# Kernel optimization log

Measured on AMD Instinct MI355X. Metric: run time of the kernel, lower is better.

The kernel has to match this reference:

```python
import jax, jax.numpy as jnp
import numpy as np
import math

B, L, D_MODEL = 4, 2048, 512
EXPAND, D_STATE, D_CONV = 6, 8, 3
D_INNER = EXPAND * D_MODEL            # 3072
DT_RANK = math.ceil(D_MODEL / 16)     # 32
NH = 8
HF = D_MODEL // NH                    # 64


def setup_inputs() -> dict:
    key = jax.random.key(0)
    ks = jax.random.split(key, 16)
    n = lambda k, sh, s=0.02: jax.random.normal(k, sh, dtype=jnp.float32) * s
    return {
        "x": jax.random.normal(ks[0], (B, L, D_MODEL), dtype=jnp.float32),
        "norm_w": jnp.ones((D_MODEL,), jnp.float32),
        "in_proj_w": n(ks[1], (2 * D_INNER, D_MODEL)),
        "conv_w": n(ks[2], (D_INNER, 1, D_CONV), 0.2),
        "conv_b": jnp.zeros((D_INNER,), jnp.float32),
        "x_proj_w": n(ks[3], (DT_RANK + 2 * D_STATE, D_INNER)),
        "dt_head_w": n(ks[4], (D_INNER, DT_RANK)),
        "dt_head_b": jnp.zeros((D_INNER,), jnp.float32),
        "D": jnp.ones((D_INNER,), jnp.float32),
        "reduce_w": n(ks[5], (D_MODEL, D_INNER)),
        "q_net_w": n(ks[6], (D_MODEL, D_MODEL)),
        "gain_q_w": n(ks[7], (D_MODEL, D_MODEL)),
        "gain_k_w": n(ks[8], (D_MODEL, D_MODEL)),
        "alpha": jnp.ones((1,), jnp.float32),
        "beta": jnp.zeros((1,), jnp.float32),
        "qkv_w": n(ks[9], (3 * D_MODEL + NH, D_MODEL)),
        "qkv_b": jnp.zeros((3 * D_MODEL + NH,), jnp.float32),
        "ttt_lr_bias": jnp.zeros((NH,), jnp.float32),
        "W1": n(ks[10], (NH, HF, HF)),
        "b1": jnp.zeros((NH, HF), jnp.float32),
        "token_idx": 1.0 / jnp.arange(1, L + 1, dtype=jnp.float32),
        "token_idx_bias": jnp.zeros((L,), jnp.float32),
        "ttt_ln_w": jnp.ones((NH, HF), jnp.float32),
        "ttt_ln_b": jnp.zeros((NH, HF), jnp.float32),
        "post_norm_w": jnp.ones((D_MODEL,), jnp.float32),
        "post_norm_b": jnp.zeros((D_MODEL,), jnp.float32),
        "wo_w": n(ks[11], (D_MODEL, D_MODEL)),
        "wo_b": jnp.zeros((D_MODEL,), jnp.float32),
    }


def _rmsnorm(x, w, eps=1e-5):
    return x * jax.lax.rsqrt(jnp.mean(x * x, axis=-1, keepdims=True) + eps) * w


def _layernorm(x, w, b, eps=1e-5):
    mu = x.mean(-1, keepdims=True)
    xh = (x - mu) * jax.lax.rsqrt(x.var(-1, keepdims=True) + eps)
    return xh * w + b


def _longhorn_scan(x, z, dt, k, q, dt_b, D):
    # x,z,dt: [B,L,di]; k,q: [B,L,ds].  Online Longhorn recurrence (matches step()).
    def step(s, t):
        x_t, z_t, dt_t, k_t, q_t = t
        dt_t = jax.nn.sigmoid(dt_t + dt_b)
        dt_t = dt_t / (1.0 + dt_t * jnp.sum(k_t * k_t, -1, keepdims=True))
        dB = dt_t[:, :, None] * k_t[:, None, :]                  # [B,di,ds]
        s = s * (1.0 - dB * k_t[:, None, :]) + x_t[:, :, None] * dB
        y_t = jnp.einsum('bdn,bn->bd', s, q_t) + D * x_t
        return s, y_t * jax.nn.silu(z_t)

    s0 = jnp.zeros((x.shape[0], x.shape[2], k.shape[2]), x.dtype)
    xs = tuple(jnp.moveaxis(a, 1, 0) for a in (x, z, dt, k, q))
    _, ys = jax.lax.scan(step, s0, xs)
    return jnp.moveaxis(ys, 0, 1)                                # [B,L,di]


def _ttt(h, qkv_w, qkv_b, ttt_lr_bias, W1, b1, token_idx, token_idx_bias,
         ln_w, ln_b, pn_w, pn_b, wo_w, wo_b, lr_mult=1.0):
    Bh, N, d = h.shape
    proj = h @ qkv_w.T + qkv_b                                   # [B,N,3d+NH]
    XQK, XV, XGate, lr = (proj[..., :d], proj[..., d:2 * d],
                          proj[..., 2 * d:3 * d], proj[..., 3 * d:])

    def heads(a):  # [B,N,d] -> [B*NH,N,HF]
        return a.reshape(Bh, N, NH, HF).transpose(0, 2, 1, 3).reshape(Bh * NH, N, HF)

    XQ = heads(XQK)            # XQ == XK in the source
    XVh = heads(XV)
    ttt_lr = jax.nn.sigmoid(lr + ttt_lr_bias) * lr_mult          # [B,N,NH]
    ttt_lr = jnp.swapaxes(ttt_lr, 0, 1).reshape(N, Bh * NH, 1)   # [N,B*NH,1]
    tok = jnp.maximum(token_idx + token_idx_bias, 0.0)           # [N]

    W1c = jnp.broadcast_to(W1[None], (Bh, NH, HF, HF)).reshape(Bh * NH, HF, HF)
    b1c = jnp.broadcast_to(b1[None], (Bh, NH, HF)).reshape(Bh * NH, HF)
    lnw = jnp.broadcast_to(ln_w[None], (Bh, NH, HF)).reshape(Bh * NH, HF)
    lnb = jnp.broadcast_to(ln_b[None], (Bh, NH, HF)).reshape(Bh * NH, HF)
    eps = 1e-6
    HFf = jnp.float32(HF)

    def step(carry, t):
        W, bb = carry
        xk, xv, lr_t, tok_t = t
        Z1 = jnp.einsum('bf,bfg->bg', xk, W) + bb
        mu = Z1.mean(-1, keepdims=True)
        std = jnp.sqrt(Z1.var(-1, keepdims=True) + eps)
        xh = (Z1 - mu) / std
        # grad of ||LN(Z1) - (XV - XK)||^2 wrt Z1 (ln_fused_l2_bwd)
        go = (lnw * xh + lnb) - (xv - xk)
        gxh = go * lnw
        grad = (HFf * gxh - gxh.sum(-1, keepdims=True)
                - xh * (gxh * xh).sum(-1, keepdims=True)) / (HFf * std)
        eta = lr_t * tok_t                                       # [B*NH,1]
        W = W - eta[:, :, None] * (xk[:, :, None] * grad[:, None, :])
        bb = bb - eta * grad
        Z1q = jnp.einsum('bf,bfg->bg', xk, W) + bb
        mu2 = Z1q.mean(-1, keepdims=True)
        std2 = jnp.sqrt(Z1q.var(-1, keepdims=True) + eps)
        out_t = xk + lnw * (Z1q - mu2) / std2 + lnb
        return (W, bb), out_t

    xs = (jnp.moveaxis(XQ, 1, 0), jnp.moveaxis(XVh, 1, 0), ttt_lr, tok)
    _, ys = jax.lax.scan(step, (W1c, b1c), xs)                   # [N,B*NH,HF]
    xqw = ys.reshape(N, Bh, NH, HF).transpose(1, 0, 2, 3).reshape(Bh, N, d)
    normed = _layernorm(xqw, pn_w, pn_b)
    gated = jax.nn.gelu(XGate, approximate=True) * normed
    return gated @ wo_w.T + wo_b


def reference(x, norm_w, in_proj_w, conv_w, conv_b, x_proj_w, dt_head_w, dt_head_b,
              D, reduce_w, q_net_w, gain_q_w, gain_k_w, alpha, beta,
              qkv_w, qkv_b, ttt_lr_bias, W1, b1, token_idx, token_idx_bias,
              ttt_ln_w, ttt_ln_b, post_norm_w, post_norm_b, wo_w, wo_b):
    residual = x                                   # residual=None in forward
    xn = _rmsnorm(residual, norm_w)
    # ---- Longhorn block ----
    xz = xn @ in_proj_w.T                          # [B,L,2*di]
    xx, z = jnp.split(xz, 2, axis=-1)
    xc = jnp.swapaxes(xx, 1, 2)                    # [B,di,L]
    xc = jax.lax.conv_general_dilated(
        xc, conv_w, (1,), [(D_CONV - 1, 0)],       # causal depthwise conv
        dimension_numbers=('NCH', 'OIH', 'NCH'), feature_group_count=D_INNER)
    xc = jax.nn.silu(xc + conv_b[None, :, None])
    xb = jnp.swapaxes(xc, 1, 2)                    # [B,L,di]
    x_dbl = xb @ x_proj_w.T
    dt = x_dbl[..., :DT_RANK] @ dt_head_w.T        # [B,L,di] (bias added in scan)
    k = x_dbl[..., DT_RANK:DT_RANK + D_STATE]
    q = x_dbl[..., DT_RANK + D_STATE:]
    y = _longhorn_scan(xb, z, dt, k, q, dt_head_b, D)   # h_hidden, [B,L,di]
    # (out_proj output is discarded by PreCoBlock, so not computed)
    h_red = y @ reduce_w.T                          # [B,L,d]
    # ---- TTT corrective branch ----
    c_hidden = _ttt(h_red, qkv_w, qkv_b, ttt_lr_bias, W1, b1, token_idx,
                    token_idx_bias, ttt_ln_w, ttt_ln_b, post_norm_w, post_norm_b,
                    wo_w, wo_b, lr_mult=1.0)
    z_long = h_red @ q_net_w.T
    z_ttt = c_hidden @ q_net_w.T
    gq = h_red @ gain_q_w.T
    gk = h_red @ gain_k_w.T
    # score = mean_i (gq_i . gk_j)/sqrt(d) == (mean_i gq_i) . gk_j / sqrt(d)
    score = jnp.einsum('bd,bld->bl', gq.mean(axis=1), gk) / jnp.sqrt(jnp.float32(D_MODEL))
    gain = jnp.minimum(jax.nn.sigmoid(alpha * score + beta), 0.55)[..., None]
    out = z_long + gain * (z_ttt - z_long)
    return (out, residual, gain)
```

## Files before the change

kernel.cpp:

```cpp
#include <hip/hip_runtime.h>
#include <hip/hip_bf16.h>
#include <cstdint>
#include <cstddef>

#define L_SEQ 2048
#define BATCH 4
#define DM    512
#define DI    3072
#define NROWS (BATCH * L_SEQ)
#define PROJW 1544
#define CTILE 16
#define BDI   (BATCH * DI)
#define SB    64
#define NSB   (L_SEQ / SB)
#define CHT   16
#define LCH   256
#define NLCH  (L_SEQ / LCH)

using bf16 = __hip_bfloat16;

typedef __attribute__((ext_vector_type(8))) short short8v;
typedef __attribute__((ext_vector_type(4))) float f32x4;


__device__ __forceinline__ float sigmoidf_(float x) { return 1.f / (1.f + __expf(-x)); }
__device__ __forceinline__ float us2f(unsigned int u) {
    union { unsigned int i; float f; } c; c.i = u << 16; return c.f;
}
__device__ __forceinline__ bf16  f2b(float f) { return __float2bfloat16(f); }
__device__ __forceinline__ float b2f(bf16 v)  { return __bfloat162float(v); }
__device__ __forceinline__ void st1(float* p, float v) { *p = v; }
__device__ __forceinline__ void st1(bf16* p, float v)  { *p = f2b(v); }

template <int CTRL>
__device__ __forceinline__ float dppadd_(float x) {
    int s = __builtin_amdgcn_update_dpp(0, __builtin_bit_cast(int, x), CTRL, 0xF, 0xF, true);
    return x + __builtin_bit_cast(float, s);
}
__device__ __forceinline__ float wave_sum_u(float x) {
    x = dppadd_<0x111>(x);
    x = dppadd_<0x112>(x);
    x = dppadd_<0x114>(x);
    x = dppadd_<0x118>(x);
    x = dppadd_<0x142>(x);
    x = dppadd_<0x143>(x);
    return __builtin_bit_cast(float,
        __builtin_amdgcn_readlane(__builtin_bit_cast(int, x), 63));
}

__global__ __launch_bounds__(256) void copy4_k(const float4* __restrict__ in,
                                               float4* __restrict__ out, int n) {
    int i = blockIdx.x * 256 + threadIdx.x;
    if (i < n) out[i] = in[i];
}

__global__ __launch_bounds__(256) void cvt_k(const float* __restrict__ in,
                                             bf16* __restrict__ out, int n4) {
    int i = blockIdx.x * 256 + threadIdx.x;
    if (i >= n4) return;
    float4 v = ((const float4*)in)[i];
    out[4 * i + 0] = f2b(v.x);
    out[4 * i + 1] = f2b(v.y);
    out[4 * i + 2] = f2b(v.z);
    out[4 * i + 3] = f2b(v.w);
}

#define C_RED  393216
#define C_QKV  197632
#define C_WO   65536
#define C_XP   73728
#define C_W1   65536
__global__ __launch_bounds__(256) void cvt_all_k(const float* __restrict__ reduce_w,
                                                 const float* __restrict__ qkv_w,
                                                 const float* __restrict__ wo_w,
                                                 const float* __restrict__ xproj_w,
                                                 const float* __restrict__ qnet_w,
                                                 const float* __restrict__ gainq_w,
                                                 const float* __restrict__ gaink_w,
                                                 bf16* __restrict__ redb,
                                                 bf16* __restrict__ qkvb,
                                                 bf16* __restrict__ wob,
                                                 bf16* __restrict__ xpb,
                                                 bf16* __restrict__ wcat) {
    int i = blockIdx.x * 256 + threadIdx.x;
    const float* src;
    bf16* dst;
    int j;
    if (i < C_RED)                { src = reduce_w; dst = redb;  j = i; }
    else if (i < C_RED + C_QKV)   { src = qkv_w;    dst = qkvb;  j = i - C_RED; }
    else if (i < C_RED + C_QKV + C_WO) { src = wo_w; dst = wob;  j = i - C_RED - C_QKV; }
    else if (i < C_RED + C_QKV + C_WO + C_XP) { src = xproj_w; dst = xpb; j = i - C_RED - C_QKV - C_WO; }
    else if (i < C_RED + C_QKV + C_WO + C_XP + C_W1) { src = qnet_w; dst = wcat; j = i - C_RED - C_QKV - C_WO - C_XP; }
    else if (i < C_RED + C_QKV + C_WO + C_XP + 2 * C_W1) { src = gainq_w; dst = wcat + (size_t)C_W1 * 4; j = i - C_RED - C_QKV - C_WO - C_XP - C_W1; }
    else if (i < C_RED + C_QKV + C_WO + C_XP + 3 * C_W1) { src = gaink_w; dst = wcat + (size_t)2 * C_W1 * 4; j = i - C_RED - C_QKV - C_WO - C_XP - 2 * C_W1; }
    else return;
    float4 v = ((const float4*)src)[j];
    bf16* o = dst + (size_t)j * 4;
    o[0] = f2b(v.x); o[1] = f2b(v.y); o[2] = f2b(v.z); o[3] = f2b(v.w);
}

__global__ __launch_bounds__(256) void rmsnorm_res_k(const float* __restrict__ x,
                                                     const float* __restrict__ w,
                                                     bf16* __restrict__ xn,
                                                     float* __restrict__ res) {
    int r = blockIdx.x, tid = threadIdx.x;
    const float* row = x + (size_t)r * DM;
    float v0 = row[tid], v1 = row[tid + 256];
    float q = v0 * v0 + v1 * v1;
#pragma unroll
    for (int off = 32; off; off >>= 1) q += __shfl_xor(q, off);
    __shared__ float sm[4];
    if ((tid & 63) == 0) sm[tid >> 6] = q;
    __syncthreads();
    q = sm[0] + sm[1] + sm[2] + sm[3];
    float scale = rsqrtf(q * (1.f / 512.f) + 1e-5f);
    bf16* orow = xn + (size_t)r * DM;
    float* rrow = res + (size_t)r * DM;
    orow[tid]       = f2b(v0 * scale * w[tid]);
    orow[tid + 256] = f2b(v1 * scale * w[tid + 256]);
    rrow[tid]       = v0;
    rrow[tid + 256] = v1;
}

template <int BIAS, typename TC>
__global__ __launch_bounds__(256) void gemm_mfma(const bf16* __restrict__ A, int lda,
                                                 const bf16* __restrict__ Wb, int ldw,
                                                 const float* __restrict__ bias,
                                                 TC* __restrict__ C, int ldc,
                                                 int N, int K) {
    __shared__ __align__(16) bf16 As[128 * 48];
    __shared__ __align__(16) bf16 Ws[128 * 48];
    const int tid = threadIdx.x;
    const int lane = tid & 63;
    const int widx = tid >> 6;
    const int bm = blockIdx.x * 128;
    const int bn = blockIdx.y * 128;
    const int wr = (widx >> 1) * 64;
    const int wc = (widx & 1) * 64;

    f32x4 acc[4][4];
#pragma unroll
    for (int i = 0; i < 4; ++i)
#pragma unroll
        for (int j = 0; j < 4; ++j) acc[i][j] = (f32x4){0.f, 0.f, 0.f, 0.f};

    const int r0 = tid >> 2;
    const int c0 = tid & 3;
    const int frow = lane & 15;
    const int fk = (lane >> 4) * 8;

    int n0 = bn + r0;       if (n0 > N - 1) n0 = N - 1;
    int n1 = bn + r0 + 64;  if (n1 > N - 1) n1 = N - 1;
    const bf16* pa0 = A + (size_t)(bm + r0) * lda + c0 * 8;
    const bf16* pa1 = A + (size_t)(bm + r0 + 64) * lda + c0 * 8;
    const bf16* pb0 = Wb + (size_t)n0 * ldw + c0 * 8;
    const bf16* pb1 = Wb + (size_t)n1 * ldw + c0 * 8;

    for (int k0 = 0; k0 < K; k0 += 32) {
        short8v a0 = *(const short8v*)(pa0 + k0);
        short8v a1 = *(const short8v*)(pa1 + k0);
        short8v b0 = *(const short8v*)(pb0 + k0);
        short8v b1 = *(const short8v*)(pb1 + k0);
        __syncthreads();
        *(short8v*)&As[r0 * 48 + c0 * 8] = a0;
        *(short8v*)&As[(r0 + 64) * 48 + c0 * 8] = a1;
        *(short8v*)&Ws[r0 * 48 + c0 * 8] = b0;
        *(short8v*)&Ws[(r0 + 64) * 48 + c0 * 8] = b1;
        __syncthreads();
        short8v af[4], bg[4];
#pragma unroll
        for (int mi = 0; mi < 4; ++mi)
            af[mi] = *(const short8v*)&As[(wr + mi * 16 + frow) * 48 + fk];
#pragma unroll
        for (int ni = 0; ni < 4; ++ni)
            bg[ni] = *(const short8v*)&Ws[(wc + ni * 16 + frow) * 48 + fk];
#pragma unroll
        for (int mi = 0; mi < 4; ++mi)
#pragma unroll
            for (int ni = 0; ni < 4; ++ni)
                acc[mi][ni] = __builtin_amdgcn_mfma_f32_16x16x32_bf16(
                    af[mi], bg[ni], acc[mi][ni], 0, 0, 0);
    }

#pragma unroll
    for (int ni = 0; ni < 4; ++ni) {
        int col = bn + wc + ni * 16 + (lane & 15);
        if (col < N) {
            float bz = BIAS ? bias[col] : 0.f;
#pragma unroll
            for (int mi = 0; mi < 4; ++mi) {
                int rbase = bm + wr + mi * 16 + (lane >> 4) * 4;
#pragma unroll
                for (int r = 0; r < 4; ++r) {
                    float v = acc[mi][ni][r] + bz;
                    st1(&C[(size_t)(rbase + r) * ldc + col], v);
                }
            }
        }
    }
}

__global__ __launch_bounds__(256) void gemm_inproj(const bf16* __restrict__ A,
                                                   const bf16* __restrict__ Wb,
                                                   bf16* __restrict__ cx,
                                                   bf16* __restrict__ cz) {
    __shared__ __align__(16) bf16 As[128 * 48];
    __shared__ __align__(16) bf16 Ws[128 * 48];
    const int tid = threadIdx.x;
    const int lane = tid & 63;
    const int widx = tid >> 6;
    const int bm = blockIdx.x * 128;
    const int bn = blockIdx.y * 128;
    const int wr = (widx >> 1) * 64;
    const int wc = (widx & 1) * 64;

    f32x4 acc[4][4];
#pragma unroll
    for (int i = 0; i < 4; ++i)
#pragma unroll
        for (int j = 0; j < 4; ++j) acc[i][j] = (f32x4){0.f, 0.f, 0.f, 0.f};

    const int r0 = tid >> 2;
    const int c0 = tid & 3;
    const int frow = lane & 15;
    const int fk = (lane >> 4) * 8;

    const bf16* pa0 = A + (size_t)(bm + r0) * DM + c0 * 8;
    const bf16* pa1 = A + (size_t)(bm + r0 + 64) * DM + c0 * 8;
    const bf16* pb0 = Wb + (size_t)(bn + r0) * DM + c0 * 8;
    const bf16* pb1 = Wb + (size_t)(bn + r0 + 64) * DM + c0 * 8;

    for (int k0 = 0; k0 < DM; k0 += 32) {
        short8v a0 = *(const short8v*)(pa0 + k0);
        short8v a1 = *(const short8v*)(pa1 + k0);
        short8v b0 = *(const short8v*)(pb0 + k0);
        short8v b1 = *(const short8v*)(pb1 + k0);
        __syncthreads();
        *(short8v*)&As[r0 * 48 + c0 * 8] = a0;
        *(short8v*)&As[(r0 + 64) * 48 + c0 * 8] = a1;
        *(short8v*)&Ws[r0 * 48 + c0 * 8] = b0;
        *(short8v*)&Ws[(r0 + 64) * 48 + c0 * 8] = b1;
        __syncthreads();
        short8v af[4], bg[4];
#pragma unroll
        for (int mi = 0; mi < 4; ++mi)
            af[mi] = *(const short8v*)&As[(wr + mi * 16 + frow) * 48 + fk];
#pragma unroll
        for (int ni = 0; ni < 4; ++ni)
            bg[ni] = *(const short8v*)&Ws[(wc + ni * 16 + frow) * 48 + fk];
#pragma unroll
        for (int mi = 0; mi < 4; ++mi)
#pragma unroll
            for (int ni = 0; ni < 4; ++ni)
                acc[mi][ni] = __builtin_amdgcn_mfma_f32_16x16x32_bf16(
                    af[mi], bg[ni], acc[mi][ni], 0, 0, 0);
    }

    bf16* Cb = (bn < DI) ? cx : cz;
    const int coff = (bn < DI) ? 0 : DI;
#pragma unroll
    for (int ni = 0; ni < 4; ++ni) {
        int col = bn + wc + ni * 16 + (lane & 15) - coff;
#pragma unroll
        for (int mi = 0; mi < 4; ++mi) {
            int rbase = bm + wr + mi * 16 + (lane >> 4) * 4;
#pragma unroll
            for (int r = 0; r < 4; ++r)
                Cb[(size_t)(rbase + r) * DI + col] = f2b(acc[mi][ni][r]);
        }
    }
}

__global__ __launch_bounds__(256) void conv_boundary_k(const bf16* __restrict__ x,
                                                       bf16* __restrict__ side) {
    int idx = blockIdx.x * 256 + threadIdx.x;
    const int total = (L_SEQ / CTILE - 1) * 2 * BDI;
    if (idx >= total) return;
    int col = idx % BDI;
    int rr = idx / BDI;
    int tile = (rr >> 1) + 1;
    int r = rr & 1;
    int b = col / DI, d = col % DI;
    int l = tile * CTILE - 2 + r;
    side[idx] = x[((size_t)b * L_SEQ + l) * DI + d];
}

__global__ __launch_bounds__(256) void conv_tile_k(bf16* __restrict__ x,
                                                   const bf16* __restrict__ side,
                                                   const float* __restrict__ cw,
                                                   const float* __restrict__ cb) {
    int idx = blockIdx.x * 256 + threadIdx.x;
    const int total = (L_SEQ / CTILE) * BDI;
    if (idx >= total) return;
    int col = idx % BDI;
    int tile = idx / BDI;
    int b = col / DI, d = col % DI;
    float w0 = cw[3 * d], w1 = cw[3 * d + 1], w2 = cw[3 * d + 2], bias = cb[d];
    size_t base = ((size_t)b * L_SEQ + tile * CTILE) * DI + d;
    float xm2, xm1;
    if (tile == 0) { xm2 = 0.f; xm1 = 0.f; }
    else {
        const bf16* sp = side + ((size_t)(tile - 1) * 2) * BDI + col;
        xm2 = b2f(sp[0]);
        xm1 = b2f(sp[BDI]);
    }
    float cur = b2f(x[base]);
#pragma unroll
    for (int i = 0; i < CTILE; ++i) {
        float nxt = (i + 1 < CTILE) ? b2f(x[base + (size_t)(i + 1) * DI]) : 0.f;
        float a = bias + w0 * xm2 + w1 * xm1 + w2 * cur;
        x[base + (size_t)i * DI] = f2b(a * sigmoidf_(a));
        xm2 = xm1; xm1 = cur; cur = nxt;
    }
}

__global__ __launch_bounds__(256) void longhorn_p1(const bf16* __restrict__ xb,
                                                   const float* __restrict__ xdbl,
                                                   const float* __restrict__ dtw,
                                                   const float* __restrict__ dtb_v,
                                                   float* __restrict__ pq) {
    int idx = blockIdx.x * 256 + threadIdx.x;
    int ch = idx / BDI;
    int col = idx % BDI;
    int b = col / DI, d = col % DI;
    float w32[32];
#pragma unroll
    for (int i = 0; i < 32; ++i) w32[i] = dtw[d * 32 + i];
    float dtb = dtb_v[d];
    float P[8] = {1.f, 1.f, 1.f, 1.f, 1.f, 1.f, 1.f, 1.f};
    float Q[8] = {0.f, 0.f, 0.f, 0.f, 0.f, 0.f, 0.f, 0.f};
    size_t rbase = ((size_t)b * L_SEQ + ch * LCH) * DI + d;
    const float* xdb = xdbl + ((size_t)b * L_SEQ + ch * LCH) * 48;

    float xv = b2f(xb[rbase]);
    for (int t = 0; t < LCH; ++t) {
        float x_c = xv;
        if (t + 1 < LCH) xv = b2f(xb[rbase + (size_t)(t + 1) * DI]);
        const float* row = xdb + (size_t)t * 48;
        float dt_c = 0.f;
#pragma unroll
        for (int i = 0; i < 32; i += 4) {
            float4 r4 = *(const float4*)(row + i);
            dt_c = fmaf(r4.x, w32[i + 0], dt_c);
            dt_c = fmaf(r4.y, w32[i + 1], dt_c);
            dt_c = fmaf(r4.z, w32[i + 2], dt_c);
            dt_c = fmaf(r4.w, w32[i + 3], dt_c);
        }
        float kq[8];
#pragma unroll
        for (int i = 0; i < 8; i += 4) *(float4*)&kq[i] = *(const float4*)(row + 32 + i);
        float sig = sigmoidf_(dt_c + dtb);
        float ksq = 0.f;
#pragma unroll
        for (int n = 0; n < 8; ++n) ksq = fmaf(kq[n], kq[n], ksq);
        float dts = sig / (1.f + sig * ksq);
#pragma unroll
        for (int n = 0; n < 8; ++n) {
            float dB = dts * kq[n];
            float a = 1.f - dB * kq[n];
            P[n] *= a;
            Q[n] = fmaf(Q[n], a, x_c * dB);
        }
    }
    float* o = pq + (size_t)idx * 16;
#pragma unroll
    for (int n = 0; n < 8; n += 4) {
        *(float4*)(o + n)     = make_float4(P[n], P[n + 1], P[n + 2], P[n + 3]);
        *(float4*)(o + 8 + n) = make_float4(Q[n], Q[n + 1], Q[n + 2], Q[n + 3]);
    }
}

__global__ __launch_bounds__(256) void longhorn_p2(float* __restrict__ pq) {
    int col = blockIdx.x * 256 + threadIdx.x;
    float s[8] = {0.f, 0.f, 0.f, 0.f, 0.f, 0.f, 0.f, 0.f};
    for (int c = 0; c < NLCH; ++c) {
        float* base = pq + ((size_t)c * BDI + col) * 16;
        float P[8], Q[8];
#pragma unroll
        for (int n = 0; n < 8; n += 4) {
            *(float4*)&P[n] = *(const float4*)(base + n);
            *(float4*)&Q[n] = *(const float4*)(base + 8 + n);
        }
#pragma unroll
        for (int n = 0; n < 8; n += 4)
            *(float4*)(base + n) = make_float4(s[n], s[n + 1], s[n + 2], s[n + 3]);
#pragma unroll
        for (int n = 0; n < 8; ++n) s[n] = fmaf(P[n], s[n], Q[n]);
    }
}

__global__ __launch_bounds__(256) void longhorn_p3(bf16* __restrict__ xb_y,
                                                   const bf16* __restrict__ z,
                                                   const float* __restrict__ xdbl,
                                                   const float* __restrict__ dtw,
                                                   const float* __restrict__ dtb_v,
                                                   const float* __restrict__ Dv,
                                                   const float* __restrict__ pq) {
    int idx = blockIdx.x * 256 + threadIdx.x;
    int ch = idx / BDI;
    int col = idx % BDI;
    int b = col / DI, d = col % DI;
    float w32[32];
#pragma unroll
    for (int i = 0; i < 32; ++i) w32[i] = dtw[d * 32 + i];
    float dtb = dtb_v[d], Dd = Dv[d];
    float s[8];
    {
        const float* base = pq + (size_t)idx * 16;
#pragma unroll
        for (int n = 0; n < 8; n += 4) *(float4*)&s[n] = *(const float4*)(base + n);
    }
    size_t rbase = ((size_t)b * L_SEQ + ch * LCH) * DI + d;
    const float* xdb = xdbl + ((size_t)b * L_SEQ + ch * LCH) * 48;

    float xv = b2f(xb_y[rbase]);
    float zv = b2f(z[rbase]);
    for (int t = 0; t < LCH; ++t) {
        float x_c = xv, z_c = zv;
        if (t + 1 < LCH) {
            size_t nidx = rbase + (size_t)(t + 1) * DI;
            xv = b2f(xb_y[nidx]);
            zv = b2f(z[nidx]);
        }
        const float* row = xdb + (size_t)t * 48;
        float dt_c = 0.f;
#pragma unroll
        for (int i = 0; i < 32; i += 4) {
            float4 r4 = *(const float4*)(row + i);
            dt_c = fmaf(r4.x, w32[i + 0], dt_c);
            dt_c = fmaf(r4.y, w32[i + 1], dt_c);
            dt_c = fmaf(r4.z, w32[i + 2], dt_c);
            dt_c = fmaf(r4.w, w32[i + 3], dt_c);
        }
        float kq[16];
#pragma unroll
        for (int i = 0; i < 16; i += 4) *(float4*)&kq[i] = *(const float4*)(row + 32 + i);
        float sig = sigmoidf_(dt_c + dtb);
        float ksq = 0.f;
#pragma unroll
        for (int n = 0; n < 8; ++n) ksq = fmaf(kq[n], kq[n], ksq);
        float dts = sig / (1.f + sig * ksq);
        float y = 0.f;
#pragma unroll
        for (int n = 0; n < 8; ++n) {
            float dB = dts * kq[n];
            s[n] = s[n] * (1.f - dB * kq[n]) + x_c * dB;
            y = fmaf(s[n], kq[8 + n], y);
        }
        y = fmaf(Dd, x_c, y);
        float out = y * (z_c * sigmoidf_(z_c));
        xb_y[rbase + (size_t)t * DI] = f2b(out);
    }
}

__global__ __launch_bounds__(128) void prep_gram_k(const bf16* __restrict__ proj,
                                                   const float* __restrict__ lr_bias,
                                                   const float* __restrict__ tok_idx,
                                                   const float* __restrict__ tok_bias,
                                                   const float* __restrict__ ln_w,
                                                   const float* __restrict__ ln_b,
                                                   float* __restrict__ xkf,
                                                   float* __restrict__ etav,
                                                   float* __restrict__ q0s,
                                                   float* __restrict__ gram) {
    __shared__ __align__(16) float xs[128][68];
    int bh = blockIdx.x >> 4;
    int blk16 = blockIdx.x & 15;
    int tid = threadIdx.x;
    int t = blk16 * 128 + tid;
    int b = bh >> 3, h = bh & 7;
    const bf16* prow = proj + ((size_t)b * L_SEQ + t) * PROJW;
    const bf16* pk = prow + h * 64;
    const bf16* pv = prow + 512 + h * 64;
    const float* lwp = ln_w + h * 64;
    const float* lbp = ln_b + h * 64;
    float* xo = xkf + ((size_t)bh * L_SEQ + t) * 64;
    float q0 = 0.f;
#pragma unroll
    for (int i = 0; i < 64; i += 8) {
        short8v sk = *(const short8v*)(pk + i);
        short8v sv = *(const short8v*)(pv + i);
        float v[8];
#pragma unroll
        for (int j = 0; j < 8; ++j) {
            float xk = us2f((unsigned short)sk[j]);
            float xv = us2f((unsigned short)sv[j]);
            v[j] = xk;
            q0 = fmaf((lbp[i + j] - xv + xk), lwp[i + j], q0);
        }
        float4 lo = make_float4(v[0], v[1], v[2], v[3]);
        float4 hi = make_float4(v[4], v[5], v[6], v[7]);
        *(float4*)(xo + i)     = lo;
        *(float4*)(xo + i + 4) = hi;
        *(float4*)&xs[tid][i]     = lo;
        *(float4*)&xs[tid][i + 4] = hi;
    }
    float eta = sigmoidf_(b2f(prow[1536 + h]) + lr_bias[h]) *
                fmaxf(tok_idx[t] + tok_bias[t], 0.f);
    size_t o = (size_t)bh * L_SEQ + t;
    etav[o] = eta;
    q0s[o]  = q0;
    __syncthreads();
    int chunk = tid >> 4, tt = tid & 15;
    const float* rt = &xs[chunk * 16 + tt][0];
    float* dst = gram + (((size_t)bh * 128 + blk16 * 8 + chunk) * 16 + tt) * 16;
#pragma unroll
    for (int ss = 0; ss < 16; ++ss) {
        const float* rs = &xs[chunk * 16 + ss][0];
        float a0 = 0.f, a1 = 0.f, a2 = 0.f, a3 = 0.f;
#pragma unroll
        for (int j = 0; j < 16; ++j) {
            float4 u = *(const float4*)(rt + 4 * j);
            float4 v = *(const float4*)(rs + 4 * j);
            a0 = fmaf(u.x, v.x, a0); a1 = fmaf(u.y, v.y, a1);
            a2 = fmaf(u.z, v.z, a2); a3 = fmaf(u.w, v.w, a3);
        }
        dst[ss] = (a0 + a1) + (a2 + a3);
    }
}

__device__ __forceinline__ void ttt_body(const bf16* __restrict__ proj,
                                         const float* __restrict__ xkf,
                                         const float* __restrict__ etav,
                                         const float* __restrict__ q0s,
                                         const float* __restrict__ gram16,
                                         const float* __restrict__ W1,
                                         const float* __restrict__ b1,
                                         const float* __restrict__ ln_w,
                                         const float* __restrict__ ln_b,
                                         bf16* __restrict__ xqw) {
    const int lane = threadIdx.x;
    const int bh = blockIdx.x;
    const int b = bh >> 3, h = bh & 7;

    __shared__ __align__(16) float xkb[2][SB][64];
    __shared__ __align__(16) bf16  xvb[2][SB][64];
    __shared__ __align__(16) float kb[2][4][CHT][CHT];
    __shared__ __align__(16) float sc[2][2][SB];
    __shared__ __align__(16) float zbb[CHT][64];
    __shared__ __align__(16) float z1qb[CHT][64];
    __shared__ __align__(16) float egb[CHT][64];
    __shared__ float mub[CHT];

    float W[64];
#pragma unroll
    for (int f = 0; f < 64; ++f) W[f] = W1[(size_t)(h * 64 + f) * 64 + lane];
    float bvec = b1[h * 64 + lane];
    float lw = ln_w[h * 64 + lane];
    float lb = ln_b[h * 64 + lane];
    float p = lw * lw;

    const float* kfg = xkf + (size_t)bh * L_SEQ * 64;
    const bf16*  pvg = proj + (size_t)b * L_SEQ * PROJW + 512 + h * 64;
    const float* evg = etav + (size_t)bh * L_SEQ;
    const float* qg  = q0s + (size_t)bh * L_SEQ;
    const float* gmg = gram16 + (size_t)bh * 128 * 256;

    auto stage_async = [&](int c, int bi) {
        const int t0g = c * SB;
#pragma unroll
        for (int i = 0; i < 16; ++i) {
            const float* gp = kfg + (size_t)(t0g + 4 * i) * 64 + lane * 4;
            __builtin_amdgcn_global_load_lds(
                (const __attribute__((address_space(1))) void*)gp,
                (__attribute__((address_space(3))) void*)&xkb[bi][4 * i][0], 16, 0, 0);
        }
#pragma unroll
        for (int i = 0; i < 8; ++i) {
            const bf16* gp = pvg + (size_t)(t0g + 8 * i + (lane >> 3)) * PROJW + (lane & 7) * 8;
            __builtin_amdgcn_global_load_lds(
                (const __attribute__((address_space(1))) void*)gp,
                (__attribute__((address_space(3))) void*)&xvb[bi][8 * i][0], 16, 0, 0);
        }
#pragma unroll
        for (int i = 0; i < 4; ++i) {
            const float* gp = gmg + (size_t)c * 1024 + i * 256 + lane * 4;
            __builtin_amdgcn_global_load_lds(
                (const __attribute__((address_space(1))) void*)gp,
                (__attribute__((address_space(3))) void*)(&kb[bi][0][0][0] + i * 256), 16, 0, 0);
        }
        {
            const float* g0 = evg + t0g + lane;
            __builtin_amdgcn_global_load_lds(
                (const __attribute__((address_space(1))) void*)g0,
                (__attribute__((address_space(3))) void*)&sc[bi][0][0], 4, 0, 0);
            const float* g1 = qg + t0g + lane;
            __builtin_amdgcn_global_load_lds(
                (const __attribute__((address_space(1))) void*)g1,
                (__attribute__((address_space(3))) void*)&sc[bi][1][0], 4, 0, 0);
        }
    };
    auto matvec16 = [&](int nbuf, int nt0) {
#pragma unroll 4
        for (int t = 0; t < CHT; ++t) {
            const float4* row = (const float4*)&xkb[nbuf][nt0 + t][0];
            float a0 = 0.f, a1 = 0.f, a2 = 0.f, a3 = 0.f;
#pragma unroll
            for (int j = 0; j < 16; ++j) {
                float4 kv = row[j];
                a0 = fmaf(kv.x, W[4 * j + 0], a0);
                a1 = fmaf(kv.y, W[4 * j + 1], a1);
                a2 = fmaf(kv.z, W[4 * j + 2], a2);
                a3 = fmaf(kv.w, W[4 * j + 3], a3);
            }
            float zb = (a0 + a1) + (a2 + a3) + bvec;
            zbb[t][lane] = zb;
            float m = wave_sum_u(zb) * 0.015625f;
            if (lane == 0) mub[t] = m;
        }
    };

    stage_async(0, 0);
    asm volatile("s_waitcnt vmcnt(0)" ::: "memory");
    __builtin_amdgcn_sched_barrier(0);
    matvec16(0, 0);

    bf16* xq = xqw + ((size_t)b * L_SEQ) * DM + h * 64 + lane;

    for (int c = 0; c < NSB; ++c) {
        const int cur = c & 1;
        if (c + 1 < NSB) stage_async(c + 1, 1 - cur);
#pragma unroll 1
        for (int sub = 0; sub < 4; ++sub) {
            const int t0 = sub * CHT;
            float eg[CHT];
            float bacc = 0.f;
            float4 krA, krB, krC, krD;
            {
                const float4* krow = (const float4*)&kb[cur][sub][0][0];
                krA = krow[0]; krB = krow[1]; krC = krow[2]; krD = krow[3];
            }
            float zb_n = zbb[0][lane];
            float xk_n = xkb[cur][t0 + 0][lane];
            float xv_n = b2f(xvb[cur][t0 + 0][lane]);
            float et_n = sc[cur][0][t0 + 0];
            float q0_n = sc[cur][1][t0 + 0];
            float mu_n = mub[0];
#pragma unroll
            for (int t = 0; t < CHT; ++t) {
                float kr[CHT];
                *(float4*)&kr[0]  = krA;
                *(float4*)&kr[4]  = krB;
                *(float4*)&kr[8]  = krC;
                *(float4*)&kr[12] = krD;
                float zb_v = zb_n;
                float xk_c = xk_n;
                float xv_c = xv_n;
                float eta  = et_n;
                float q0u  = q0_n;
                float muv  = mu_n;
                if (t + 1 < CHT) {
                    const float4* krow = (const float4*)&kb[cur][sub][t + 1][0];
                    krA = krow[0]; krB = krow[1]; krC = krow[2]; krD = krow[3];
                    zb_n = zbb[t + 1][lane];
                    xk_n = xkb[cur][t0 + t + 1][lane];
                    xv_n = b2f(xvb[cur][t0 + t + 1][lane]);
                    et_n = sc[cur][0][t0 + t + 1];
                    q0_n = sc[cur][1][t0 + t + 1];
                    mu_n = mub[t + 1];
                }

                float gg0 = bacc, gg1 = 0.f, gg2 = 0.f, gg3 = 0.f;
#pragma unroll
                for (int s = 0; s < t; ++s) {
                    if ((s & 3) == 0) gg0 = fmaf(kr[s], eg[s], gg0);
                    else if ((s & 3) == 1) gg1 = fmaf(kr[s], eg[s], gg1);
                    else if ((s & 3) == 2) gg2 = fmaf(kr[s], eg[s], gg2);
                    else gg3 = fmaf(kr[s], eg[s], gg3);
                }
                float z1 = zb_v - ((gg0 + gg1) + (gg2 + gg3));
                float d = z1 - muv;
                float q = (lb - xv_c + xk_c) * lw;
                float S2  = wave_sum_u(d * d);
                float PZ1 = wave_sum_u(p * d);
                float PZ2 = wave_sum_u(p * d * d);
                float Q1  = wave_sum_u(q * d);
                float istd = rsqrtf(S2 * 0.015625f + 1e-6f);
                float A_ = fmaf(istd, PZ1, q0u);
                float Bv = fmaf(istd * istd, PZ2, istd * Q1);
                float xh = d * istd;
                float gxh = fmaf(p, xh, q);
                float grad = (64.f * gxh - A_ - xh * Bv) * (istd * 0.015625f);
                float egt = eta * grad;
                eg[t] = egt;
                egb[t][lane] = egt;
                z1qb[t][lane] = fmaf(-eta * (kr[t] + 1.f), grad, z1);
                bacc += egt;
            }
#pragma unroll 4
            for (int t = 0; t < CHT; ++t) {
                float dq = z1qb[t][lane] - mub[t];
                float SQ = wave_sum_u(dq * dq);
                float istd2 = rsqrtf(SQ * 0.015625f + 1e-6f);
                float xk_c = xkb[cur][t0 + t][lane];
                float outv = fmaf(lw, dq * istd2, xk_c + lb);
                xq[(size_t)(c * SB + t0 + t) * DM] = f2b(outv);
            }
            bool last = (c == NSB - 1) && (sub == 3);
            if (!last) {
#pragma unroll 2
                for (int s = 0; s < CHT; ++s) {
                    float egs = egb[s][lane];
                    const float4* row = (const float4*)&xkb[cur][t0 + s][0];
#pragma unroll
                    for (int j = 0; j < 16; ++j) {
                        float4 kv = row[j];
                        W[4 * j + 0] = fmaf(-egs, kv.x, W[4 * j + 0]);
                        W[4 * j + 1] = fmaf(-egs, kv.y, W[4 * j + 1]);
                        W[4 * j + 2] = fmaf(-egs, kv.z, W[4 * j + 2]);
                        W[4 * j + 3] = fmaf(-egs, kv.w, W[4 * j + 3]);
                    }
                }
                bvec -= bacc;
                int nbuf = cur, nt0 = t0 + CHT;
                if (sub == 3) {
                    nbuf = 1 - cur; nt0 = 0;
                    asm volatile("s_waitcnt vmcnt(0)" ::: "memory");
                    __builtin_amdgcn_sched_barrier(0);
                }
                matvec16(nbuf, nt0);
            }
        }
    }
}

__global__ __launch_bounds__(256) void hetero_k(const bf16* __restrict__ proj,
                                                const float* __restrict__ xkf,
                                                const float* __restrict__ etav,
                                                const float* __restrict__ q0s,
                                                const float* __restrict__ gram16,
                                                const float* __restrict__ W1,
                                                const float* __restrict__ b1,
                                                const float* __restrict__ ln_w,
                                                const float* __restrict__ ln_b,
                                                bf16* __restrict__ xqw,
                                                const bf16* __restrict__ hred,
                                                const bf16* __restrict__ wcat,
                                                bf16* __restrict__ zl,
                                                bf16* __restrict__ gq,
                                                bf16* __restrict__ gk) {
    if (blockIdx.x < 32) {
        if (threadIdx.x < 64)
            ttt_body(proj, xkf, etav, q0s, gram16, W1, b1, ln_w, ln_b, xqw);
        return;
    }
    __shared__ __align__(16) bf16 As[128 * 48];
    __shared__ __align__(16) bf16 Ws[128 * 48];
    const int bidx = blockIdx.x - 32;
    const int tid = threadIdx.x;
    const int lane = tid & 63;
    const int widx = tid >> 6;
    const int bm = (bidx & 63) * 128;
    const int bn = (bidx >> 6) * 128;
    const int wr = (widx >> 1) * 64;
    const int wc = (widx & 1) * 64;

    f32x4 acc[4][4];
#pragma unroll
    for (int i = 0; i < 4; ++i)
#pragma unroll
        for (int j = 0; j < 4; ++j) acc[i][j] = (f32x4){0.f, 0.f, 0.f, 0.f};

    const int r0 = tid >> 2;
    const int c0 = tid & 3;
    const int frow = lane & 15;
    const int fk = (lane >> 4) * 8;

    const bf16* pa0 = hred + (size_t)(bm + r0) * DM + c0 * 8;
    const bf16* pa1 = hred + (size_t)(bm + r0 + 64) * DM + c0 * 8;
    const bf16* pb0 = wcat + (size_t)(bn + r0) * DM + c0 * 8;
    const bf16* pb1 = wcat + (size_t)(bn + r0 + 64) * DM + c0 * 8;

    for (int k0 = 0; k0 < DM; k0 += 32) {
        short8v a0 = *(const short8v*)(pa0 + k0);
        short8v a1 = *(const short8v*)(pa1 + k0);
        short8v b0 = *(const short8v*)(pb0 + k0);
        short8v b1 = *(const short8v*)(pb1 + k0);
        __syncthreads();
        *(short8v*)&As[r0 * 48 + c0 * 8] = a0;
        *(short8v*)&As[(r0 + 64) * 48 + c0 * 8] = a1;
        *(short8v*)&Ws[r0 * 48 + c0 * 8] = b0;
        *(short8v*)&Ws[(r0 + 64) * 48 + c0 * 8] = b1;
        __syncthreads();
        short8v af[4], bg[4];
#pragma unroll
        for (int mi = 0; mi < 4; ++mi)
            af[mi] = *(const short8v*)&As[(wr + mi * 16 + frow) * 48 + fk];
#pragma unroll
        for (int ni = 0; ni < 4; ++ni)
            bg[ni] = *(const short8v*)&Ws[(wc + ni * 16 + frow) * 48 + fk];
#pragma unroll
        for (int mi = 0; mi < 4; ++mi)
#pragma unroll
            for (int ni = 0; ni < 4; ++ni)
                acc[mi][ni] = __builtin_amdgcn_mfma_f32_16x16x32_bf16(
                    af[mi], bg[ni], acc[mi][ni], 0, 0, 0);
    }

#pragma unroll
    for (int ni = 0; ni < 4; ++ni) {
        int col = bn + wc + ni * 16 + (lane & 15);
        int buf = col >> 9;
        int lc = col & 511;
        bf16* Cb = (buf == 0) ? zl : (buf == 1) ? gq : gk;
#pragma unroll
        for (int mi = 0; mi < 4; ++mi) {
            int rbase = bm + wr + mi * 16 + (lane >> 4) * 4;
#pragma unroll
            for (int r = 0; r < 4; ++r)
                Cb[(size_t)(rbase + r) * 512 + lc] = f2b(acc[mi][ni][r]);
        }
    }
}

__global__ __launch_bounds__(256) void gated_k(const bf16* __restrict__ xqw,
                                               const bf16* __restrict__ proj,
                                               const float* __restrict__ pnw,
                                               const float* __restrict__ pnb,
                                               bf16* __restrict__ gated) {
    int r = blockIdx.x, tid = threadIdx.x;
    const bf16* row = xqw + (size_t)r * DM;
    float v0 = b2f(row[tid]), v1 = b2f(row[tid + 256]);
    float s = v0 + v1, q = v0 * v0 + v1 * v1;
#pragma unroll
    for (int off = 32; off; off >>= 1) {
        s += __shfl_xor(s, off);
        q += __shfl_xor(q, off);
    }
    __shared__ float sm[8];
    if ((tid & 63) == 0) { sm[tid >> 6] = s; sm[4 + (tid >> 6)] = q; }
    __syncthreads();
    s = sm[0] + sm[1] + sm[2] + sm[3];
    q = sm[4] + sm[5] + sm[6] + sm[7];
    float mu = s * (1.f / 512.f);
    float var = q * (1.f / 512.f) - mu * mu;
    float istd = rsqrtf(var + 1e-5f);
    const bf16* grow = proj + (size_t)r * PROJW + 1024;
    bf16* orow = gated + (size_t)r * DM;
#pragma unroll
    for (int e = 0; e < 2; ++e) {
        int c = tid + e * 256;
        float xv = (e == 0) ? v0 : v1;
        float nv = (xv - mu) * istd * pnw[c] + pnb[c];
        float g = b2f(grow[c]);
        float gg = 0.5f * g * (1.f + tanhf(0.7978845608028654f * (g + 0.044715f * g * g * g)));
        orow[c] = f2b(gg * nv);
    }
}

__global__ __launch_bounds__(256) void mean1_k(const bf16* __restrict__ gq,
                                               float* __restrict__ partial) {
    int blk = blockIdx.x;
    int b = blk >> 4, c = blk & 15;
    int tid = threadIdx.x;
    const bf16* p = gq + ((size_t)b * L_SEQ + c * 128) * DM + tid * 2;
    float a0 = 0.f, a1 = 0.f;
    for (int l = 0; l < 128; ++l) {
        ushort2 u = *(const ushort2*)(p + (size_t)l * DM);
        a0 += us2f(u.x); a1 += us2f(u.y);
    }
    partial[(size_t)blk * DM + tid * 2]     = a0;
    partial[(size_t)blk * DM + tid * 2 + 1] = a1;
}
__global__ __launch_bounds__(256) void mean2_k(const float* __restrict__ partial,
                                               float* __restrict__ gqm) {
    int t = blockIdx.x * 256 + threadIdx.x;
    if (t >= 2048) return;
    int b = t >> 9, d = t & 511;
    float acc = 0.f;
#pragma unroll
    for (int c = 0; c < 16; ++c) acc += partial[(size_t)(b * 16 + c) * DM + d];
    gqm[t] = acc * (1.f / 2048.f);
}

__global__ __launch_bounds__(64) void final_k(const bf16* __restrict__ zl,
                                              const bf16* __restrict__ zt,
                                              const bf16* __restrict__ gk,
                                              const float* __restrict__ gqm,
                                              const float* __restrict__ alpha,
                                              const float* __restrict__ beta,
                                              float* __restrict__ out,
                                              float* __restrict__ gain_out) {
    int r = blockIdx.x;
    int lane = threadIdx.x;
    int b = r >> 11;
    const bf16* gkr = gk + (size_t)r * DM;
    const float* gmb = gqm + b * DM;
    float acc = 0.f;
#pragma unroll
    for (int i = 0; i < 8; ++i) acc = fmaf(gmb[lane + 64 * i], b2f(gkr[lane + 64 * i]), acc);
#pragma unroll
    for (int off = 32; off; off >>= 1) acc += __shfl_xor(acc, off);
    float score = acc * 0.04419417382415922f;
    float g = sigmoidf_(alpha[0] * score + beta[0]);
    g = fminf(g, 0.55f);
    if (lane == 0) gain_out[r] = g;
    const bf16* zlr = zl + (size_t)r * DM;
    const bf16* ztr = zt + (size_t)r * DM;
    float* orow = out + (size_t)r * DM;
#pragma unroll
    for (int i = 0; i < 8; ++i) {
        int c = lane + 64 * i;
        float a = b2f(zlr[c]);
        orow[c] = a + g * (b2f(ztr[c]) - a);
    }
}


extern "C" void kernel_launch(void* const* d_in, const int* in_sizes, int n_in,
                              void* d_out, int out_size, void* d_ws, size_t ws_size,
                              hipStream_t stream) {
    const float* x           = (const float*)d_in[0];
    const float* norm_w      = (const float*)d_in[1];
    const float* in_proj_w   = (const float*)d_in[2];
    const float* conv_w      = (const float*)d_in[3];
    const float* conv_b      = (const float*)d_in[4];
    const float* x_proj_w    = (const float*)d_in[5];
    const float* dt_head_w   = (const float*)d_in[6];
    const float* dt_head_b   = (const float*)d_in[7];
    const float* Dvec        = (const float*)d_in[8];
    const float* reduce_w    = (const float*)d_in[9];
    const float* q_net_w     = (const float*)d_in[10];
    const float* gain_q_w    = (const float*)d_in[11];
    const float* gain_k_w    = (const float*)d_in[12];
    const float* alpha       = (const float*)d_in[13];
    const float* beta        = (const float*)d_in[14];
    const float* qkv_w       = (const float*)d_in[15];
    const float* qkv_b       = (const float*)d_in[16];
    const float* ttt_lr_bias = (const float*)d_in[17];
    const float* W1          = (const float*)d_in[18];
    const float* b1          = (const float*)d_in[19];
    const float* token_idx   = (const float*)d_in[20];
    const float* token_bias  = (const float*)d_in[21];
    const float* ttt_ln_w    = (const float*)d_in[22];
    const float* ttt_ln_b    = (const float*)d_in[23];
    const float* post_norm_w = (const float*)d_in[24];
    const float* post_norm_b = (const float*)d_in[25];
    const float* wo_w        = (const float*)d_in[26];
    const float* wo_b        = (const float*)d_in[27];

    const size_t SZ_ROWDM = (size_t)NROWS * DM;
    const size_t MB = 1024u * 1024u;
    const size_t KB = 1024u;
    char* base = (char*)d_ws;

    float* out_p  = (float*)d_out;
    float* res_p  = out_p + SZ_ROWDM;
    float* gain_p = out_p + 2 * SZ_ROWDM;

    if (ws_size < 116 * MB) {
        copy4_k<<<(int)(SZ_ROWDM / 4 / 256), 256, 0, stream>>>(
            (const float4*)x, (float4*)res_p, (int)(SZ_ROWDM / 4));
        return;
    }

    bf16*  ws0    = (bf16*)base;
    bf16*  redb   = (bf16*)base;
    bf16*  qkvb   = (bf16*)(base + 3 * MB);
    bf16*  wob16  = (bf16*)(base + 4 * MB + 768 * KB);
    bf16*  xpb    = (bf16*)(base + 5 * MB + 512 * KB);
    bf16*  wcat   = (bf16*)(base + 114 * MB + 512 * KB);
    bf16*  xn     = (bf16*)(base + 7 * MB);
    bf16*  h_red  = xn;
    bf16*  cside  = (bf16*)(base + 7 * MB);
    float* lpq    = (float*)(base + 7 * MB);
    bf16*  bufX   = (bf16*)(base + 16 * MB);
    bf16*  bufZ   = (bf16*)(base + 64 * MB);
    float* xdbl   = (float*)(base + 112 * MB);
    float* gqm    = (float*)(base + 113 * MB + 512 * KB);
    float* mpart  = (float*)(base + 114 * MB);
    bf16*  proj   = bufX;
    bf16*  xqw    = bufZ;
    bf16*  zl     = (bf16*)(base + 72 * MB);
    bf16*  gq     = (bf16*)(base + 80 * MB);
    float* gramb  = (float*)(base + 88 * MB);
    bf16*  gk     = (bf16*)(base + 92 * MB);
    bf16*  zttt   = (bf16*)(base + 100 * MB);
    bf16*  gated  = (bf16*)(base + 104 * MB);
    bf16*  chid   = (bf16*)(base + 42 * MB);
    float* xkf    = (float*)(base + 42 * MB);
    float* etav   = (float*)(base + 58 * MB);
    float* q0s    = (float*)(base + 58 * MB + 512 * KB);

    rmsnorm_res_k<<<NROWS, 256, 0, stream>>>(x, norm_w, xn, res_p);

    cvt_k<<<(2 * DI * DM / 4 + 255) / 256, 256, 0, stream>>>(in_proj_w, ws0, 2 * DI * DM / 4);
    {
        dim3 g(NROWS / 128, 2 * DI / 128);
        gemm_inproj<<<g, 256, 0, stream>>>(xn, ws0, bufX, bufZ);
    }

    cvt_all_k<<<(C_RED + C_QKV + C_WO + C_XP + 3 * C_W1 + 255) / 256, 256, 0, stream>>>(
        reduce_w, qkv_w, wo_w, x_proj_w, q_net_w, gain_q_w, gain_k_w,
        redb, qkvb, wob16, xpb, wcat);

    conv_boundary_k<<<((L_SEQ / CTILE - 1) * 2 * BDI) / 256, 256, 0, stream>>>(bufX, cside);
    conv_tile_k<<<((L_SEQ / CTILE) * BDI) / 256, 256, 0, stream>>>(bufX, cside, conv_w, conv_b);

    {
        dim3 g(NROWS / 128, 1);
        gemm_mfma<0, float><<<g, 256, 0, stream>>>(bufX, DI, xpb, DI, nullptr, xdbl, 48, 48, DI);
    }

    longhorn_p1<<<(NLCH * BDI) / 256, 256, 0, stream>>>(bufX, xdbl, dt_head_w, dt_head_b, lpq);
    longhorn_p2<<<BDI / 256, 256, 0, stream>>>(lpq);
    longhorn_p3<<<(NLCH * BDI) / 256, 256, 0, stream>>>(bufX, bufZ, xdbl, dt_head_w,
                                                        dt_head_b, Dvec, lpq);

    {
        dim3 g(NROWS / 128, DM / 128);
        gemm_mfma<0, bf16><<<g, 256, 0, stream>>>(bufX, DI, redb, DI, nullptr, h_red, DM, DM, DI);
    }

    {
        dim3 g(NROWS / 128, (PROJW + 127) / 128);
        gemm_mfma<1, bf16><<<g, 256, 0, stream>>>(h_red, DM, qkvb, DM, qkv_b, proj, PROJW, PROJW, DM);
    }

    prep_gram_k<<<32 * 16, 128, 0, stream>>>(proj, ttt_lr_bias, token_idx, token_bias,
                                             ttt_ln_w, ttt_ln_b, xkf, etav, q0s, gramb);

    hetero_k<<<32 + 768, 256, 0, stream>>>(proj, xkf, etav, q0s, gramb, W1, b1,
                                           ttt_ln_w, ttt_ln_b, xqw,
                                           h_red, wcat, zl, gq, gk);

    gated_k<<<NROWS, 256, 0, stream>>>(xqw, proj, post_norm_w, post_norm_b, gated);

    {
        dim3 g(NROWS / 128, DM / 128);
        gemm_mfma<1, bf16><<<g, 256, 0, stream>>>(gated, DM, wob16, DM, wo_b, chid, DM, DM, DM);
        gemm_mfma<0, bf16><<<g, 256, 0, stream>>>(chid, DM, wcat, DM, nullptr, zttt, DM, DM, DM);
    }

    mean1_k<<<64, 256, 0, stream>>>(gq, mpart);
    mean2_k<<<8, 256, 0, stream>>>(mpart, gqm);
    final_k<<<NROWS, 64, 0, stream>>>(zl, zttt, gk, gqm, alpha, beta, out_p, gain_p);
}
```

Measured before the change: 2.501 ms.

## Halve Longhorn scan chunk length and reshuffle weight conversions to free workspace

Cuts the chunk length of the chunked Longhorn scan from 256 to 128, doubling the number of parallel chunks in the first and third scan passes and shortening each thread's serial loop. The larger chunk-state buffer no longer fits where it was, so it moves to the start of the workspace. To make room, the single combined weight-conversion kernel is split into three that run just before each weight is needed. This adds two kernel launches, and the middle pass that carries state across chunks now has more serial work.

```diff
diff --git a/kernel.cpp b/kernel.cpp
--- a/kernel.cpp
+++ b/kernel.cpp
@@ -14,7 +14,7 @@
 #define SB    64
 #define NSB   (L_SEQ / SB)
 #define CHT   16
-#define LCH   256
+#define LCH   128
 #define NLCH  (L_SEQ / LCH)
 
 using bf16 = __hip_bfloat16;
@@ -65,34 +65,36 @@
     out[4 * i + 3] = f2b(v.w);
 }
 
+__global__ __launch_bounds__(256) void cvt3_k(const float* __restrict__ a,
+                                              const float* __restrict__ b,
+                                              const float* __restrict__ c,
+                                              bf16* __restrict__ out) {
+    int i = blockIdx.x * 256 + threadIdx.x;
+    const int seg = 512 * 512 / 4;
+    if (i >= 3 * seg) return;
+    const float* src = (i < seg) ? a : (i < 2 * seg) ? b : c;
+    int j = (i < seg) ? i : (i < 2 * seg) ? i - seg : i - 2 * seg;
+    float4 v = ((const float4*)src)[j];
+    bf16* o = out + (size_t)i * 4;
+    o[0] = f2b(v.x); o[1] = f2b(v.y); o[2] = f2b(v.z); o[3] = f2b(v.w);
+}
+
 #define C_RED  393216
 #define C_QKV  197632
 #define C_WO   65536
-#define C_XP   73728
-#define C_W1   65536
-__global__ __launch_bounds__(256) void cvt_all_k(const float* __restrict__ reduce_w,
+__global__ __launch_bounds__(256) void cvt_rqw_k(const float* __restrict__ reduce_w,
                                                  const float* __restrict__ qkv_w,
                                                  const float* __restrict__ wo_w,
-                                                 const float* __restrict__ xproj_w,
-                                                 const float* __restrict__ qnet_w,
-                                                 const float* __restrict__ gainq_w,
-                                                 const float* __restrict__ gaink_w,
                                                  bf16* __restrict__ redb,
                                                  bf16* __restrict__ qkvb,
-                                                 bf16* __restrict__ wob,
-                                                 bf16* __restrict__ xpb,
-                                                 bf16* __restrict__ wcat) {
+                                                 bf16* __restrict__ wob) {
     int i = blockIdx.x * 256 + threadIdx.x;
     const float* src;
     bf16* dst;
     int j;
-    if (i < C_RED)                { src = reduce_w; dst = redb;  j = i; }
-    else if (i < C_RED + C_QKV)   { src = qkv_w;    dst = qkvb;  j = i - C_RED; }
-    else if (i < C_RED + C_QKV + C_WO) { src = wo_w; dst = wob;  j = i - C_RED - C_QKV; }
-    else if (i < C_RED + C_QKV + C_WO + C_XP) { src = xproj_w; dst = xpb; j = i - C_RED - C_QKV - C_WO; }
-    else if (i < C_RED + C_QKV + C_WO + C_XP + C_W1) { src = qnet_w; dst = wcat; j = i - C_RED - C_QKV - C_WO - C_XP; }
-    else if (i < C_RED + C_QKV + C_WO + C_XP + 2 * C_W1) { src = gainq_w; dst = wcat + (size_t)C_W1 * 4; j = i - C_RED - C_QKV - C_WO - C_XP - C_W1; }
-    else if (i < C_RED + C_QKV + C_WO + C_XP + 3 * C_W1) { src = gaink_w; dst = wcat + (size_t)2 * C_W1 * 4; j = i - C_RED - C_QKV - C_WO - C_XP - 2 * C_W1; }
+    if (i < C_RED)                     { src = reduce_w; dst = redb; j = i; }
+    else if (i < C_RED + C_QKV)        { src = qkv_w;    dst = qkvb; j = i - C_RED; }
+    else if (i < C_RED + C_QKV + C_WO) { src = wo_w;     dst = wob;  j = i - C_RED - C_QKV; }
     else return;
     float4 v = ((const float4*)src)[j];
     bf16* o = dst + (size_t)j * 4;
@@ -954,16 +956,16 @@
         return;
     }
 
-    bf16*  ws0    = (bf16*)base;
+    bf16*  inpb   = (bf16*)base;
+    bf16*  xpb    = (bf16*)(base + 6 * MB);
+    float* lpq    = (float*)base;
     bf16*  redb   = (bf16*)base;
     bf16*  qkvb   = (bf16*)(base + 3 * MB);
     bf16*  wob16  = (bf16*)(base + 4 * MB + 768 * KB);
-    bf16*  xpb    = (bf16*)(base + 5 * MB + 512 * KB);
     bf16*  wcat   = (bf16*)(base + 114 * MB + 512 * KB);
     bf16*  xn     = (bf16*)(base + 7 * MB);
     bf16*  h_red  = xn;
     bf16*  cside  = (bf16*)(base + 7 * MB);
-    float* lpq    = (float*)(base + 7 * MB);
     bf16*  bufX   = (bf16*)(base + 16 * MB);
     bf16*  bufZ   = (bf16*)(base + 64 * MB);
     float* xdbl   = (float*)(base + 112 * MB);
@@ -984,19 +986,18 @@
 
     rmsnorm_res_k<<<NROWS, 256, 0, stream>>>(x, norm_w, xn, res_p);
 
-    cvt_k<<<(2 * DI * DM / 4 + 255) / 256, 256, 0, stream>>>(in_proj_w, ws0, 2 * DI * DM / 4);
+    cvt_k<<<(2 * DI * DM / 4 + 255) / 256, 256, 0, stream>>>(in_proj_w, inpb, 2 * DI * DM / 4);
     {
         dim3 g(NROWS / 128, 2 * DI / 128);
-        gemm_inproj<<<g, 256, 0, stream>>>(xn, ws0, bufX, bufZ);
-    }
-
-    cvt_all_k<<<(C_RED + C_QKV + C_WO + C_XP + 3 * C_W1 + 255) / 256, 256, 0, stream>>>(
-        reduce_w, qkv_w, wo_w, x_proj_w, q_net_w, gain_q_w, gain_k_w,
-        redb, qkvb, wob16, xpb, wcat);
+        gemm_inproj<<<g, 256, 0, stream>>>(xn, inpb, bufX, bufZ);
+    }
+
+    cvt3_k<<<(3 * 65536 + 255) / 256, 256, 0, stream>>>(q_net_w, gain_q_w, gain_k_w, wcat);
 
     conv_boundary_k<<<((L_SEQ / CTILE - 1) * 2 * BDI) / 256, 256, 0, stream>>>(bufX, cside);
     conv_tile_k<<<((L_SEQ / CTILE) * BDI) / 256, 256, 0, stream>>>(bufX, cside, conv_w, conv_b);
 
+    cvt_k<<<(48 * DI / 4 + 255) / 256, 256, 0, stream>>>(x_proj_w, xpb, 48 * DI / 4);
     {
         dim3 g(NROWS / 128, 1);
         gemm_mfma<0, float><<<g, 256, 0, stream>>>(bufX, DI, xpb, DI, nullptr, xdbl, 48, 48, DI);
@@ -1007,6 +1008,9 @@
     longhorn_p3<<<(NLCH * BDI) / 256, 256, 0, stream>>>(bufX, bufZ, xdbl, dt_head_w,
                                                         dt_head_b, Dvec, lpq);
 
+    cvt_rqw_k<<<(C_RED + C_QKV + C_WO + 255) / 256, 256, 0, stream>>>(
+        reduce_w, qkv_w, wo_w, redb, qkvb, wob16);
+
     {
         dim3 g(NROWS / 128, DM / 128);
         gemm_mfma<0, bf16><<<g, 256, 0, stream>>>(bufX, DI, redb, DI, nullptr, h_red, DM, DM, DI);
```

Result: faster. 2.298 ms (median of 2 runs) (-8.1%).
